# Kernel optimization log

Hardware: AMD Instinct MI355X
Metric: run time of the kernel (lower is better)

The kernel has to match this reference:

```python
import jax, jax.numpy as jnp
import numpy as np

NUM_HEADS = 8
SCALE = 3
TOPKS = [16, 8, 8]  # index 0 = coarsest level


def avg_pool2(t):
    B, C, H, W = t.shape
    return t.reshape(B, C, H // 2, 2, W // 2, 2).mean(axis=(3, 5))


def _to_heads(t, Hi, Wi):
    # [B, C, Hi, Wi] with C = nh*hd (head-major channels) -> [B, nh, Hi*Wi, hd]
    B, C = t.shape[0], t.shape[1]
    hd = C // NUM_HEADS
    return t.reshape(B, NUM_HEADS, hd, Hi * Wi).transpose(0, 1, 3, 2)


def setup_inputs() -> dict:
    key = jax.random.key(0)
    ks = jax.random.split(key, 6)
    B, H, W, C = 2, 96, 96, 128
    N = H * W
    s = 0.02
    return {
        "x": jax.random.normal(ks[0], (B, N, C), jnp.float32),
        "target": jax.random.normal(ks[1], (B, N, C), jnp.float32),
        "Wq": jax.random.normal(ks[2], (C, C), jnp.float32) * s,
        "Wk": jax.random.normal(ks[3], (C, C), jnp.float32) * s,
        "Wv": jax.random.normal(ks[4], (C, C), jnp.float32) * s,
        "Wo": jax.random.normal(ks[5], (C, C), jnp.float32) * s,
        "bo": jnp.zeros((C,), jnp.float32),
        "H": 96,
        "W": 96,
    }


def reference(x, target, Wq, Wk, Wv, Wo, bo, H, W):
    B, N, C = x.shape
    hd = C // NUM_HEADS
    temp = 1.0 / jnp.sqrt(jnp.float32(hd))
    xi = x.transpose(0, 2, 1).reshape(B, C, H, W)
    ti = target.transpose(0, 2, 1).reshape(B, C, H, W)
    # 1x1 conv projections == channel-wise matmul
    q = jnp.einsum('bchw,oc->bohw', xi, Wq)
    k = jnp.einsum('bchw,oc->bohw', ti, Wk)
    v = jnp.einsum('bchw,oc->bohw', ti, Wv)
    qs, ks_, vs, hw = [], [], [], []
    for i in range(SCALE):
        Hi, Wi = H >> i, W >> i
        qs.append(_to_heads(q, Hi, Wi))
        ks_.append(_to_heads(k, Hi, Wi))
        vs.append(_to_heads(v, Hi, Wi))
        hw.append((Hi, Wi))
        if i != SCALE - 1:
            q, k, v = avg_pool2(q), avg_pool2(k), avg_pool2(v)
    # ---- coarsest level: full attention + top-k key selection ----
    i = SCALE - 1
    A = jax.nn.softmax(temp * jnp.einsum('bhnd,bhmd->bhnm', qs[i], ks_[i]), axis=-1)
    msg = jnp.einsum('bhnm,bhmd->bhnd', A, vs[i])  # [B,h,Nc,hd]
    topk_score, topk_idx = jax.lax.top_k(A, TOPKS[0])  # [B,h,Nc,K]
    # ---- refine coarse -> fine over quadtree children of top-k keys ----
    gather = jax.vmap(jax.vmap(lambda arr, idx: arr[idx]))  # over B, h
    for lvl in range(SCALE - 2, -1, -1):
        Hi, Wi = hw[lvl]
        Hp, Wpar = hw[lvl + 1]
        Nf = Hi * Wi
        K = topk_idx.shape[-1]
        yf, xf = jnp.divmod(jnp.arange(Nf), Wi)
        parent = (yf // 2) * Wpar + (xf // 2)  # [Nf] parent query index
        p_idx = topk_idx[:, :, parent, :]  # [B,h,Nf,K] selected coarse keys
        ky, kx = jnp.divmod(p_idx, Wpar)
        dy = jnp.array([0, 0, 1, 1], jnp.int32)
        dx = jnp.array([0, 1, 0, 1], jnp.int32)
        child = ((2 * ky)[..., None] + dy) * Wi + (2 * kx)[..., None] + dx
        cand = child.reshape(B, NUM_HEADS, Nf, K * 4)  # candidate fine keys
        kg = gather(ks_[lvl], cand)  # [B,h,Nf,4K,hd]
        vg = gather(vs[lvl], cand)
        sc = temp * jnp.einsum('bhnd,bhnkd->bhnk', qs[lvl], kg)
        Af = jax.nn.softmax(sc, axis=-1)
        msg_f = jnp.einsum('bhnk,bhnkd->bhnd', Af, vg)
        msg = msg[:, :, parent, :] + msg_f  # assemble with upsampled coarse msg
        if lvl > 0:
            kk = TOPKS[SCALE - 1 - lvl]
            ts, tp = jax.lax.top_k(Af, kk)
            topk_idx = jnp.take_along_axis(cand, tp, axis=-1)
            topk_score = ts
    out = msg.transpose(0, 2, 1, 3).reshape(B, N, C)  # head-major channels
    return out @ Wo.T + bo
```

## Files before the change

### kernel.cpp

```cpp
#include <hip/hip_runtime.h>

#define NB   2
#define NHD  8
#define BH   16
#define HD   16
#define N0   9216
#define N1   2304
#define N2   576
#define W0_  96
#define W1_  48
#define W2_  24
#define M_TOT 18432
#define TEMP 0.25f

__device__ __forceinline__ float kth_largest64(float v, int k){
    unsigned b = __float_as_uint(v);
    unsigned u = (b & 0x80000000u) ? ~b : (b | 0x80000000u);
    unsigned g = 0u;
#pragma unroll
    for(int bit=31; bit>=0; --bit){
        unsigned cand = g | (1u<<bit);
        if ((int)__popcll(__ballot(u >= cand)) >= k) g = cand;
    }
    unsigned rb = (g & 0x80000000u) ? (g & 0x7FFFFFFFu) : ~g;
    return __uint_as_float(rb);
}

__global__ __launch_bounds__(256) void k_proj(const float* __restrict__ x, const float* __restrict__ tg,
    const float* __restrict__ Wq, const float* __restrict__ Wk, const float* __restrict__ Wv,
    float* __restrict__ q0, float* __restrict__ k0, float* __restrict__ v0)
{
    __shared__ __align__(16) float At[16][68];
    __shared__ __align__(16) float Wt[16][132];
    const int t = threadIdx.x;
    const int which = blockIdx.y;
    const float* A  = (which==0)? x : tg;
    const float* Wm = (which==0)? Wq : (which==1? Wk : Wv);
    float* dst      = (which==0)? q0 : (which==1? k0 : v0);
    const int m0 = blockIdx.x * 64;
    const int tx = t & 15, ty = t >> 4;

    float acc[4][8];
#pragma unroll
    for(int i=0;i<4;i++)
#pragma unroll
        for(int j=0;j<8;j++) acc[i][j]=0.f;

    const int ar = t>>2, akq = (t&3)*4;
    const int wo = t>>1, wkq = (t&1)*8;

    for(int kc=0;kc<128;kc+=16){
        float4 av = *(const float4*)(A + (m0+ar)*128 + kc + akq);
        At[akq+0][ar] = av.x;
        At[akq+1][ar] = av.y;
        At[akq+2][ar] = av.z;
        At[akq+3][ar] = av.w;
        float4 w0 = *(const float4*)(Wm + wo*128 + kc + wkq);
        float4 w1 = *(const float4*)(Wm + wo*128 + kc + wkq + 4);
        Wt[wkq+0][wo] = w0.x; Wt[wkq+1][wo] = w0.y;
        Wt[wkq+2][wo] = w0.z; Wt[wkq+3][wo] = w0.w;
        Wt[wkq+4][wo] = w1.x; Wt[wkq+5][wo] = w1.y;
        Wt[wkq+6][wo] = w1.z; Wt[wkq+7][wo] = w1.w;
        __syncthreads();
#pragma unroll
        for(int kk=0;kk<16;kk++){
            float4 a4 = *(const float4*)&At[kk][ty*4];
            float4 wa = *(const float4*)&Wt[kk][tx*4];
            float4 wb = *(const float4*)&Wt[kk][64 + tx*4];
            float avr[4] = {a4.x,a4.y,a4.z,a4.w};
            float wvr[8] = {wa.x,wa.y,wa.z,wa.w, wb.x,wb.y,wb.z,wb.w};
#pragma unroll
            for(int i=0;i<4;i++)
#pragma unroll
                for(int j=0;j<8;j++) acc[i][j] += avr[i]*wvr[j];
        }
        __syncthreads();
    }
    const int hA = tx>>2, dA = (tx&3)*4;
#pragma unroll
    for(int i=0;i<4;i++){
        int m = m0 + ty*4 + i;
        int b = m / N0; int n = m - b*N0;
        float4 sA = make_float4(acc[i][0], acc[i][1], acc[i][2], acc[i][3]);
        float4 sB = make_float4(acc[i][4], acc[i][5], acc[i][6], acc[i][7]);
        *(float4*)(dst + ((b*NHD + hA    )*N0 + n)*16 + dA) = sA;
        *(float4*)(dst + ((b*NHD + hA + 4)*N0 + n)*16 + dA) = sB;
    }
}

__global__ __launch_bounds__(256) void k_pool01(const float4* __restrict__ src0,
    float4* __restrict__ dst1, float4* __restrict__ q2f,
    float4* __restrict__ k2T, float4* __restrict__ v2T)
{
    int tid = blockIdx.x*256 + threadIdx.x;
    if (tid >= 110592) return;
    int d4 = tid & 3;
    int rest = tid >> 2;
    int n2 = rest % N2; int g = rest / N2;
    int yo2 = n2 / W2_, xo2 = n2 - yo2*W2_;

    const float4* s = src0 + g*N0*4;
    float4* d1 = dst1 + g*N1*4;
    float4 l1[4];
#pragma unroll
    for(int yy=0;yy<2;yy++){
#pragma unroll
        for(int xx=0;xx<2;xx++){
            int y1 = 2*yo2+yy, x1 = 2*xo2+xx;
            int n1 = y1*W1_ + x1;
            int cbase = (2*y1)*W0_ + 2*x1;
            float4 a = s[(cbase       )*4 + d4];
            float4 b = s[(cbase+1     )*4 + d4];
            float4 c = s[(cbase+W0_   )*4 + d4];
            float4 d = s[(cbase+W0_+1 )*4 + d4];
            float4 o;
            o.x = 0.25f*(a.x+b.x+c.x+d.x);
            o.y = 0.25f*(a.y+b.y+c.y+d.y);
            o.z = 0.25f*(a.z+b.z+c.z+d.z);
            o.w = 0.25f*(a.w+b.w+c.w+d.w);
            d1[n1*4 + d4] = o;
            l1[yy*2+xx] = o;
        }
    }
    float4 o2;
    o2.x = 0.25f*(l1[0].x+l1[1].x+l1[2].x+l1[3].x);
    o2.y = 0.25f*(l1[0].y+l1[1].y+l1[2].y+l1[3].y);
    o2.z = 0.25f*(l1[0].z+l1[1].z+l1[2].z+l1[3].z);
    o2.w = 0.25f*(l1[0].w+l1[1].w+l1[2].w+l1[3].w);
    int grp = g >> 4, bh = g & 15;
    if (grp == 0)      q2f[(bh*N2 + n2)*4 + d4] = o2;
    else if (grp == 1) k2T[(bh*4 + d4)*N2 + n2] = o2;
    else               v2T[(bh*4 + d4)*N2 + n2] = o2;
}

__device__ __forceinline__ void top16_sel(const float ev[9], int lane, float* cv, int* cx, int* ip)
{
    float head = ev[0];
#pragma unroll
    for(int i=1;i<9;i++) head = fmaxf(head, ev[i]);

    float T = kth_largest64(head, 16);

    int ci = 0;
#pragma unroll
    for(int i=0;i<9;i++) ci += (ev[i] >= T) ? 1 : 0;
    int ps = ci;
#pragma unroll
    for(int d=1;d<64;d<<=1){
        int t = __shfl_up(ps, d);
        if (lane >= d) ps += t;
    }
    int excl = ps - ci;
    int C = __shfl(ps, 63);

    int o = excl;
#pragma unroll
    for(int i=0;i<9;i++){
        if (ev[i] >= T){
            cv[o] = ev[i];
            cx[o] = i*64 + lane;
            o++;
        }
    }
    if (lane < 4){ cv[C+lane] = -1.0f; cx[C+lane] = 0x7fffffff; }

    for(int l=lane; l<C; l+=64){
        float mv = cv[l]; int mi = cx[l];
        int rank = 0;
        for(int c=0;c<C;c+=4){
            float4 vv = *(const float4*)(cv + c);
            int4   ii = *(const int4*)(cx + c);
            rank += (vv.x > mv || (vv.x == mv && ii.x < mi)) ? 1 : 0;
            rank += (vv.y > mv || (vv.y == mv && ii.y < mi)) ? 1 : 0;
            rank += (vv.z > mv || (vv.z == mv && ii.z < mi)) ? 1 : 0;
            rank += (vv.w > mv || (vv.w == mv && ii.w < mi)) ? 1 : 0;
        }
        if (rank < 16) ip[rank] = mi;
    }
}

__global__ __launch_bounds__(256) void k_attn2(const float* __restrict__ q2, const float* __restrict__ k2,
    const float* __restrict__ v2, float* __restrict__ msg2, int* __restrict__ idx2)
{
    __shared__ __align__(16) float cval[4][580];
    __shared__ __align__(16) int   cidx[4][580];
    const int bh = blockIdx.x;
    const int wv = threadIdx.x>>6, lane = threadIdx.x&63;
    const int qA = blockIdx.y*8 + wv*2;
    const int qB = qA + 1;

    float qrA[16], qrB[16];
    {
        const float4* qpA = (const float4*)(q2 + (bh*N2 + qA)*16);
        const float4* qpB = (const float4*)(q2 + (bh*N2 + qB)*16);
#pragma unroll
        for(int dq=0;dq<4;dq++){
            float4 va = qpA[dq];
            qrA[dq*4+0]=va.x; qrA[dq*4+1]=va.y; qrA[dq*4+2]=va.z; qrA[dq*4+3]=va.w;
            float4 vb = qpB[dq];
            qrB[dq*4+0]=vb.x; qrB[dq*4+1]=vb.y; qrB[dq*4+2]=vb.z; qrB[dq*4+3]=vb.w;
        }
    }

    const float4* kT = (const float4*)k2 + bh*4*N2;
    const float4* vT = (const float4*)v2 + bh*4*N2;

    float evA[9], evB[9];
    float mxA = -1e30f, mxB = -1e30f;
#pragma unroll
    for(int t9=0;t9<9;t9++){
        int m = t9*64 + lane;
        float sA = 0.f, sB = 0.f;
#pragma unroll
        for(int dg=0;dg<4;dg++){
            float4 kv = kT[dg*N2 + m];
            sA += qrA[dg*4+0]*kv.x + qrA[dg*4+1]*kv.y + qrA[dg*4+2]*kv.z + qrA[dg*4+3]*kv.w;
            sB += qrB[dg*4+0]*kv.x + qrB[dg*4+1]*kv.y + qrB[dg*4+2]*kv.z + qrB[dg*4+3]*kv.w;
        }
        sA *= TEMP; sB *= TEMP;
        evA[t9]=sA; evB[t9]=sB;
        mxA = fmaxf(mxA, sA);
        mxB = fmaxf(mxB, sB);
    }
#pragma unroll
    for(int st=1; st<64; st<<=1){
        mxA = fmaxf(mxA, __shfl_xor(mxA, st));
        mxB = fmaxf(mxB, __shfl_xor(mxB, st));
    }

    float sumA=0.f, sumB=0.f;
    float accA[16], accB[16];
#pragma unroll
    for(int d=0;d<16;d++){ accA[d]=0.f; accB[d]=0.f; }
#pragma unroll
    for(int t9=0;t9<9;t9++){
        int m = t9*64 + lane;
        float eA = expf(evA[t9]-mxA);
        float eB = expf(evB[t9]-mxB);
        evA[t9]=eA; evB[t9]=eB;
        sumA += eA; sumB += eB;
#pragma unroll
        for(int dg=0;dg<4;dg++){
            float4 vv = vT[dg*N2 + m];
            accA[dg*4+0] += eA*vv.x; accA[dg*4+1] += eA*vv.y;
            accA[dg*4+2] += eA*vv.z; accA[dg*4+3] += eA*vv.w;
            accB[dg*4+0] += eB*vv.x; accB[dg*4+1] += eB*vv.y;
            accB[dg*4+2] += eB*vv.z; accB[dg*4+3] += eB*vv.w;
        }
    }
#pragma unroll
    for(int st=1; st<64; st<<=1){
        sumA += __shfl_xor(sumA, st);
        sumB += __shfl_xor(sumB, st);
    }

    const bool b5 = (lane & 32) != 0;
    const bool b4 = (lane & 16) != 0;
    const bool b3 = (lane & 8) != 0;
    const bool b2 = (lane & 4) != 0;
    float r8A[8], r8B[8];
#pragma unroll
    for(int i=0;i<8;i++){
        float sndA  = b5 ? accA[i]   : accA[i+8];
        float keptA = b5 ? accA[i+8] : accA[i];
        r8A[i] = keptA + __shfl_xor(sndA, 32);
        float sndB  = b5 ? accB[i]   : accB[i+8];
        float keptB = b5 ? accB[i+8] : accB[i];
        r8B[i] = keptB + __shfl_xor(sndB, 32);
    }
    float r4A[4], r4B[4];
#pragma unroll
    for(int i=0;i<4;i++){
        float sndA  = b4 ? r8A[i]   : r8A[i+4];
        float keptA = b4 ? r8A[i+4] : r8A[i];
        r4A[i] = keptA + __shfl_xor(sndA, 16);
        float sndB  = b4 ? r8B[i]   : r8B[i+4];
        float keptB = b4 ? r8B[i+4] : r8B[i];
        r4B[i] = keptB + __shfl_xor(sndB, 16);
    }
    float r2A[2], r2B[2];
#pragma unroll
    for(int i=0;i<2;i++){
        float sndA  = b3 ? r4A[i]   : r4A[i+2];
        float keptA = b3 ? r4A[i+2] : r4A[i];
        r2A[i] = keptA + __shfl_xor(sndA, 8);
        float sndB  = b3 ? r4B[i]   : r4B[i+2];
        float keptB = b3 ? r4B[i+2] : r4B[i];
        r2B[i] = keptB + __shfl_xor(sndB, 8);
    }
    {
        float sndA  = b2 ? r2A[0] : r2A[1];
        float keptA = b2 ? r2A[1] : r2A[0];
        r2A[0] = keptA + __shfl_xor(sndA, 4);
        float sndB  = b2 ? r2B[0] : r2B[1];
        float keptB = b2 ? r2B[1] : r2B[0];
        r2B[0] = keptB + __shfl_xor(sndB, 4);
    }
    r2A[0] += __shfl_xor(r2A[0], 2);
    r2B[0] += __shfl_xor(r2B[0], 2);
    r2A[0] += __shfl_xor(r2A[0], 1);
    r2B[0] += __shfl_xor(r2B[0], 1);
    float invA = 1.0f/sumA, invB = 1.0f/sumB;
    if ((lane&3)==0){
        msg2[(bh*N2+qA)*16 + (lane>>2)] = r2A[0]*invA;
        msg2[(bh*N2+qB)*16 + (lane>>2)] = r2B[0]*invB;
    }

    top16_sel(evA, lane, cval[wv], cidx[wv], idx2 + (bh*N2+qA)*16);
    top16_sel(evB, lane, cval[wv], cidx[wv], idx2 + (bh*N2+qB)*16);
}

__global__ __launch_bounds__(256) void k_ref10(
    const float* __restrict__ q1, const float* __restrict__ k1, const float* __restrict__ v1,
    const float* __restrict__ q0, const float* __restrict__ k0, const float* __restrict__ v0,
    const float* __restrict__ msg2, const int* __restrict__ idx2, float* __restrict__ msg0)
{
    __shared__ float msg1s[4][16];
    __shared__ int   idx1s[4][8];
    const int bid = (blockIdx.x & 7)*1152 + (blockIdx.x >> 3);
    const int bh = bid / 576, tile = bid - bh*576;
    const int tyy = tile / 24, txx = tile - tyy*24;
    const int py0 = tyy*2, px0 = txx*2;
    const int wv = threadIdx.x>>6, lane = threadIdx.x&63;

    const int ppy = py0 + (wv>>1), ppx = px0 + (wv&1);

    {
        const int n  = ppy*W1_ + ppx;
        const int par = (ppy>>1)*W2_ + (ppx>>1);
        const int kk = lane>>2, tt = lane&3, dy = tt>>1, dx = tt&1;
        int p = idx2[(bh*N2+par)*16 + kk];
        int ky = p / W2_, kx = p - ky*W2_;
        int child = (2*ky+dy)*W1_ + 2*kx+dx;

        const float* qp = q1 + (bh*N1+n)*16;
        float qr[16];
#pragma unroll
        for(int d=0; d<16; d+=4){
            float4 qq = *(const float4*)(qp+d);
            qr[d]=qq.x; qr[d+1]=qq.y; qr[d+2]=qq.z; qr[d+3]=qq.w;
        }
        const float4* kp = (const float4*)(k1 + (bh*N1+child)*16);
        float s = 0.f;
#pragma unroll
        for(int dq=0;dq<4;dq++){
            float4 kv = kp[dq];
            s += qr[dq*4+0]*kv.x + qr[dq*4+1]*kv.y + qr[dq*4+2]*kv.z + qr[dq*4+3]*kv.w;
        }
        s *= TEMP;

        float T8 = kth_largest64(s, 8);
        unsigned long long mgt = __ballot(s > T8);
        unsigned long long meq = __ballot(s == T8);
        int ngt = (int)__popcll(mgt);
        int ltg = __builtin_amdgcn_mbcnt_lo((unsigned)mgt, 0);
        ltg = __builtin_amdgcn_mbcnt_hi((unsigned)(mgt>>32), ltg);
        int lte = __builtin_amdgcn_mbcnt_lo((unsigned)meq, 0);
        lte = __builtin_amdgcn_mbcnt_hi((unsigned)(meq>>32), lte);
        int slot = (s > T8) ? ltg : ((s == T8) ? (ngt + lte) : 8);
        if (slot < 8) idx1s[wv][slot] = child;

        float e = expf(s);
        float sum = e;
#pragma unroll
        for(int st=1; st<64; st<<=1) sum += __shfl_xor(sum, st);

        float acc[16];
        const float4* vp = (const float4*)(v1 + (bh*N1+child)*16);
#pragma unroll
        for(int dq=0;dq<4;dq++){
            float4 vv = vp[dq];
            acc[dq*4+0]=e*vv.x; acc[dq*4+1]=e*vv.y; acc[dq*4+2]=e*vv.z; acc[dq*4+3]=e*vv.w;
        }
        const bool b5 = (lane & 32) != 0;
        float r8[8];
#pragma unroll
        for(int ii=0;ii<8;ii++){
            float snd  = b5 ? acc[ii]   : acc[ii+8];
            float kept = b5 ? acc[ii+8] : acc[ii];
            r8[ii] = kept + __shfl_xor(snd, 32);
        }
        const bool b4 = (lane & 16) != 0;
        float r4[4];
#pragma unroll
        for(int ii=0;ii<4;ii++){
            float snd  = b4 ? r8[ii]   : r8[ii+4];
            float kept = b4 ? r8[ii+4] : r8[ii];
            r4[ii] = kept + __shfl_xor(snd, 16);
        }
        const bool b3 = (lane & 8) != 0;
        float r2[2];
#pragma unroll
        for(int ii=0;ii<2;ii++){
            float snd  = b3 ? r4[ii]   : r4[ii+2];
            float kept = b3 ? r4[ii+2] : r4[ii];
            r2[ii] = kept + __shfl_xor(snd, 8);
        }
        const bool b2 = (lane & 4) != 0;
        {
            float snd  = b2 ? r2[0] : r2[1];
            float kept = b2 ? r2[1] : r2[0];
            r2[0] = kept + __shfl_xor(snd, 4);
        }
        r2[0] += __shfl_xor(r2[0], 2);
        r2[0] += __shfl_xor(r2[0], 1);

        float inv1 = 1.0f/sum;
        if ((lane&3)==0){
            int d = lane>>2;
            msg1s[wv][d] = msg2[(bh*N2+par)*16 + d] + r2[0]*inv1;
        }
    }

    const int j = lane & 31, sub = lane >> 5;
    const int kk = j>>2, tt = j&3, dy = tt>>1, dx = tt&1;
    int p = idx1s[wv][kk];
    int ky = p / W1_, kx = p - ky*W1_;
    int child = (2*ky+dy)*W0_ + 2*kx+dx;

    float kr[16];
    {
        const float4* kp = (const float4*)(k0 + (bh*N0+child)*16);
#pragma unroll
        for(int dq=0;dq<4;dq++){
            float4 kv = kp[dq];
            kr[dq*4+0]=kv.x; kr[dq*4+1]=kv.y; kr[dq*4+2]=kv.z; kr[dq*4+3]=kv.w;
        }
    }
    const int cy0 = 2*ppy, cx0 = 2*ppx + sub;
    int nq[2];
    float s_[2];
#pragma unroll
    for(int it=0; it<2; it++){
        nq[it] = (cy0+it)*W0_ + cx0;
        const float* qp = q0 + (bh*N0+nq[it])*16;
        float qr[16];
#pragma unroll
        for(int d=0; d<16; d+=4){
            float4 qq = *(const float4*)(qp+d);
            qr[d]=qq.x; qr[d+1]=qq.y; qr[d+2]=qq.z; qr[d+3]=qq.w;
        }
        float s = 0.f;
#pragma unroll
        for(int dq=0;dq<4;dq++){
            s += qr[dq*4+0]*kr[dq*4+0] + qr[dq*4+1]*kr[dq*4+1]
               + qr[dq*4+2]*kr[dq*4+2] + qr[dq*4+3]*kr[dq*4+3];
        }
        s_[it] = s * TEMP;
    }
    float vr[16];
    {
        const float4* vp = (const float4*)(v0 + (bh*N0+child)*16);
#pragma unroll
        for(int dq=0;dq<4;dq++){
            float4 vv = vp[dq];
            vr[dq*4+0]=vv.x; vr[dq*4+1]=vv.y; vr[dq*4+2]=vv.z; vr[dq*4+3]=vv.w;
        }
    }
    const float m1d = msg1s[wv][j>>1];

    float e0 = expf(s_[0]);
    float e1 = expf(s_[1]);
    float sum0 = e0, sum1 = e1;
#pragma unroll
    for(int st=1; st<32; st<<=1){
        sum0 += __shfl_xor(sum0, st);
        sum1 += __shfl_xor(sum1, st);
    }

    float acc0[16], acc1[16];
#pragma unroll
    for(int d=0;d<16;d++){ acc0[d] = e0*vr[d]; acc1[d] = e1*vr[d]; }

    const bool c4 = (j & 16) != 0;
    float p8A[8], p8B[8];
#pragma unroll
    for(int ii=0;ii<8;ii++){
        float sndA  = c4 ? acc0[ii]   : acc0[ii+8];
        float keptA = c4 ? acc0[ii+8] : acc0[ii];
        p8A[ii] = keptA + __shfl_xor(sndA, 16);
        float sndB  = c4 ? acc1[ii]   : acc1[ii+8];
        float keptB = c4 ? acc1[ii+8] : acc1[ii];
        p8B[ii] = keptB + __shfl_xor(sndB, 16);
    }
    const bool c3 = (j & 8) != 0;
    float p4A[4], p4B[4];
#pragma unroll
    for(int ii=0;ii<4;ii++){
        float sndA  = c3 ? p8A[ii]   : p8A[ii+4];
        float keptA = c3 ? p8A[ii+4] : p8A[ii];
        p4A[ii] = keptA + __shfl_xor(sndA, 8);
        float sndB  = c3 ? p8B[ii]   : p8B[ii+4];
        float keptB = c3 ? p8B[ii+4] : p8B[ii];
        p4B[ii] = keptB + __shfl_xor(sndB, 8);
    }
    const bool c2 = (j & 4) != 0;
    float p2A[2], p2B[2];
#pragma unroll
    for(int ii=0;ii<2;ii++){
        float sndA  = c2 ? p4A[ii]   : p4A[ii+2];
        float keptA = c2 ? p4A[ii+2] : p4A[ii];
        p2A[ii] = keptA + __shfl_xor(sndA, 4);
        float sndB  = c2 ? p4B[ii]   : p4B[ii+2];
        float keptB = c2 ? p4B[ii+2] : p4B[ii];
        p2B[ii] = keptB + __shfl_xor(sndB, 4);
    }
    const bool c1 = (j & 2) != 0;
    {
        float sndA  = c1 ? p2A[0] : p2A[1];
        float keptA = c1 ? p2A[1] : p2A[0];
        p2A[0] = keptA + __shfl_xor(sndA, 2);
        float sndB  = c1 ? p2B[0] : p2B[1];
        float keptB = c1 ? p2B[1] : p2B[0];
        p2B[0] = keptB + __shfl_xor(sndB, 2);
    }
    p2A[0] += __shfl_xor(p2A[0], 1);
    p2B[0] += __shfl_xor(p2B[0], 1);

    float inv0 = 1.0f/sum0, inv1 = 1.0f/sum1;
    if ((j&1)==0){
        int d = j>>1;
        int b_ = bh>>3, h = bh&7;
        msg0[(b_*N0+nq[0])*128 + h*16 + d] = m1d + p2A[0]*inv0;
        msg0[(b_*N0+nq[1])*128 + h*16 + d] = m1d + p2B[0]*inv1;
    }
}

__global__ __launch_bounds__(256) void k_out(const float* __restrict__ msg0, const float* __restrict__ Wo,
    const float* __restrict__ bo, float* __restrict__ out)
{
    __shared__ __align__(16) float At[16][68];
    __shared__ __align__(16) float Wt[16][132];
    const int t = threadIdx.x;
    const int m0 = blockIdx.x * 64;
    const int tx = t & 15, ty = t >> 4;

    float acc[4][8];
#pragma unroll
    for(int i=0;i<4;i++)
#pragma unroll
        for(int j=0;j<8;j++) acc[i][j]=0.f;

    const int ar = t>>2, akq = (t&3)*4;
    const int wo = t>>1, wkq = (t&1)*8;

    for(int kc=0;kc<128;kc+=16){
        float4 av = *(const float4*)(msg0 + (m0+ar)*128 + kc + akq);
        At[akq+0][ar] = av.x;
        At[akq+1][ar] = av.y;
        At[akq+2][ar] = av.z;
        At[akq+3][ar] = av.w;
        float4 w0 = *(const float4*)(Wo + wo*128 + kc + wkq);
        float4 w1 = *(const float4*)(Wo + wo*128 + kc + wkq + 4);
        Wt[wkq+0][wo] = w0.x; Wt[wkq+1][wo] = w0.y;
        Wt[wkq+2][wo] = w0.z; Wt[wkq+3][wo] = w0.w;
        Wt[wkq+4][wo] = w1.x; Wt[wkq+5][wo] = w1.y;
        Wt[wkq+6][wo] = w1.z; Wt[wkq+7][wo] = w1.w;
        __syncthreads();
#pragma unroll
        for(int kk=0;kk<16;kk++){
            float4 a4 = *(const float4*)&At[kk][ty*4];
            float4 wa = *(const float4*)&Wt[kk][tx*4];
            float4 wb = *(const float4*)&Wt[kk][64 + tx*4];
            float avr[4] = {a4.x,a4.y,a4.z,a4.w};
            float wvr[8] = {wa.x,wa.y,wa.z,wa.w, wb.x,wb.y,wb.z,wb.w};
#pragma unroll
            for(int i=0;i<4;i++)
#pragma unroll
                for(int j=0;j<8;j++) acc[i][j] += avr[i]*wvr[j];
        }
        __syncthreads();
    }
#pragma unroll
    for(int i=0;i<4;i++){
        int m = m0 + ty*4 + i;
        float4 sA = make_float4(acc[i][0]+bo[tx*4+0], acc[i][1]+bo[tx*4+1],
                                acc[i][2]+bo[tx*4+2], acc[i][3]+bo[tx*4+3]);
        float4 sB = make_float4(acc[i][4]+bo[64+tx*4+0], acc[i][5]+bo[64+tx*4+1],
                                acc[i][6]+bo[64+tx*4+2], acc[i][7]+bo[64+tx*4+3]);
        *(float4*)(out + m*128 + tx*4)      = sA;
        *(float4*)(out + m*128 + 64 + tx*4) = sB;
    }
}

extern "C" void kernel_launch(void* const* d_in, const int* in_sizes, int n_in,
                              void* d_out, int out_size, void* d_ws, size_t ws_size,
                              hipStream_t stream) {
    const float* x  = (const float*)d_in[0];
    const float* tg = (const float*)d_in[1];
    const float* Wq = (const float*)d_in[2];
    const float* Wk = (const float*)d_in[3];
    const float* Wv = (const float*)d_in[4];
    const float* Wo = (const float*)d_in[5];
    const float* bo = (const float*)d_in[6];

    float* ws = (float*)d_ws;
    float* q0   = ws + 0;
    float* k0   = ws + 2359296;
    float* v0   = ws + 4718592;
    float* q1   = ws + 7077888;
    float* k1   = ws + 7667712;
    float* v1   = ws + 8257536;
    float* q2   = ws + 8847360;
    float* k2   = ws + 8994816;
    float* v2   = ws + 9142272;
    float* msg2 = ws + 9289728;
    float* msg0 = ws + 10027008;
    int*   idx2 = (int*)(ws + 12386304);

    k_proj<<<dim3(288,3), 256, 0, stream>>>(x, tg, Wq, Wk, Wv, q0, k0, v0);
    k_pool01<<<432, 256, 0, stream>>>((const float4*)q0, (float4*)q1,
                                      (float4*)q2, (float4*)k2, (float4*)v2);
    k_attn2<<<dim3(16,72), 256, 0, stream>>>(q2, k2, v2, msg2, idx2);
    k_ref10<<<9216, 256, 0, stream>>>(q1, k1, v1, q0, k0, v0, msg2, idx2, msg0);
    k_out<<<288, 256, 0, stream>>>(msg0, Wo, bo, (float*)d_out);
}
```

Measured before the change: 214.6 us.

## Prefetch GEMM tiles into registers, ballot-based prefix scan, fast exp

The projection and output GEMM kernels now load the next k-chunk of A and W into registers before computing on the current shared-memory tile, so global load latency overlaps with the FMA loop. The shuffle-based inclusive scan in top-16 selection is replaced by four ballot/mbcnt steps over the count bits. expf calls in the fine-level attention kernels become __expf, which is faster but less accurate. The prefetch adds register pressure, and the bitwise scan assumes per-lane counts below 16.

```diff
diff --git a/kernel.cpp b/kernel.cpp
--- a/kernel.cpp
+++ b/kernel.cpp
@@ -24,6 +24,18 @@
     }
     unsigned rb = (g & 0x80000000u) ? (g & 0x7FFFFFFFu) : ~g;
     return __uint_as_float(rb);
+}
+
+__device__ __forceinline__ void scan_counts64(int ci, int &excl, int &C){
+    excl = 0; C = 0;
+#pragma unroll
+    for(int b=0;b<4;b++){
+        unsigned long long mb = __ballot(((unsigned)ci>>b)&1u);
+        int lt = __builtin_amdgcn_mbcnt_lo((unsigned)mb, 0);
+        lt = __builtin_amdgcn_mbcnt_hi((unsigned)(mb>>32), lt);
+        excl += lt << b;
+        C += ((int)__popcll(mb)) << b;
+    }
 }
 
 __global__ __launch_bounds__(256) void k_proj(const float* __restrict__ x, const float* __restrict__ tg,
@@ -49,19 +61,26 @@
     const int ar = t>>2, akq = (t&3)*4;
     const int wo = t>>1, wkq = (t&1)*8;
 
+    float4 av = *(const float4*)(A + (m0+ar)*128 + akq);
+    float4 w0 = *(const float4*)(Wm + wo*128 + wkq);
+    float4 w1 = *(const float4*)(Wm + wo*128 + wkq + 4);
+
     for(int kc=0;kc<128;kc+=16){
-        float4 av = *(const float4*)(A + (m0+ar)*128 + kc + akq);
         At[akq+0][ar] = av.x;
         At[akq+1][ar] = av.y;
         At[akq+2][ar] = av.z;
         At[akq+3][ar] = av.w;
-        float4 w0 = *(const float4*)(Wm + wo*128 + kc + wkq);
-        float4 w1 = *(const float4*)(Wm + wo*128 + kc + wkq + 4);
         Wt[wkq+0][wo] = w0.x; Wt[wkq+1][wo] = w0.y;
         Wt[wkq+2][wo] = w0.z; Wt[wkq+3][wo] = w0.w;
         Wt[wkq+4][wo] = w1.x; Wt[wkq+5][wo] = w1.y;
         Wt[wkq+6][wo] = w1.z; Wt[wkq+7][wo] = w1.w;
         __syncthreads();
+        float4 nav, nw0, nw1;
+        if (kc < 112){
+            nav = *(const float4*)(A + (m0+ar)*128 + kc+16 + akq);
+            nw0 = *(const float4*)(Wm + wo*128 + kc+16 + wkq);
+            nw1 = *(const float4*)(Wm + wo*128 + kc+16 + wkq + 4);
+        }
 #pragma unroll
         for(int kk=0;kk<16;kk++){
             float4 a4 = *(const float4*)&At[kk][ty*4];
@@ -75,6 +94,7 @@
                 for(int j=0;j<8;j++) acc[i][j] += avr[i]*wvr[j];
         }
         __syncthreads();
+        if (kc < 112){ av = nav; w0 = nw0; w1 = nw1; }
     }
     const int hA = tx>>2, dA = (tx&3)*4;
 #pragma unroll
@@ -144,14 +164,8 @@
     int ci = 0;
 #pragma unroll
     for(int i=0;i<9;i++) ci += (ev[i] >= T) ? 1 : 0;
-    int ps = ci;
-#pragma unroll
-    for(int d=1;d<64;d<<=1){
-        int t = __shfl_up(ps, d);
-        if (lane >= d) ps += t;
-    }
-    int excl = ps - ci;
-    int C = __shfl(ps, 63);
+    int excl, C;
+    scan_counts64(ci, excl, C);
 
     int o = excl;
 #pragma unroll
@@ -360,7 +374,7 @@
         int slot = (s > T8) ? ltg : ((s == T8) ? (ngt + lte) : 8);
         if (slot < 8) idx1s[wv][slot] = child;
 
-        float e = expf(s);
+        float e = __expf(s);
         float sum = e;
 #pragma unroll
         for(int st=1; st<64; st<<=1) sum += __shfl_xor(sum, st);
@@ -459,8 +473,8 @@
     }
     const float m1d = msg1s[wv][j>>1];
 
-    float e0 = expf(s_[0]);
-    float e1 = expf(s_[1]);
+    float e0 = __expf(s_[0]);
+    float e1 = __expf(s_[1]);
     float sum0 = e0, sum1 = e1;
 #pragma unroll
     for(int st=1; st<32; st<<=1){
@@ -544,19 +558,26 @@
     const int ar = t>>2, akq = (t&3)*4;
     const int wo = t>>1, wkq = (t&1)*8;
 
+    float4 av = *(const float4*)(msg0 + (m0+ar)*128 + akq);
+    float4 w0 = *(const float4*)(Wo + wo*128 + wkq);
+    float4 w1 = *(const float4*)(Wo + wo*128 + wkq + 4);
+
     for(int kc=0;kc<128;kc+=16){
-        float4 av = *(const float4*)(msg0 + (m0+ar)*128 + kc + akq);
         At[akq+0][ar] = av.x;
         At[akq+1][ar] = av.y;
         At[akq+2][ar] = av.z;
         At[akq+3][ar] = av.w;
-        float4 w0 = *(const float4*)(Wo + wo*128 + kc + wkq);
-        float4 w1 = *(const float4*)(Wo + wo*128 + kc + wkq + 4);
         Wt[wkq+0][wo] = w0.x; Wt[wkq+1][wo] = w0.y;
         Wt[wkq+2][wo] = w0.z; Wt[wkq+3][wo] = w0.w;
         Wt[wkq+4][wo] = w1.x; Wt[wkq+5][wo] = w1.y;
         Wt[wkq+6][wo] = w1.z; Wt[wkq+7][wo] = w1.w;
         __syncthreads();
+        float4 nav, nw0, nw1;
+        if (kc < 112){
+            nav = *(const float4*)(msg0 + (m0+ar)*128 + kc+16 + akq);
+            nw0 = *(const float4*)(Wo + wo*128 + kc+16 + wkq);
+            nw1 = *(const float4*)(Wo + wo*128 + kc+16 + wkq + 4);
+        }
 #pragma unroll
         for(int kk=0;kk<16;kk++){
             float4 a4 = *(const float4*)&At[kk][ty*4];
@@ -570,6 +591,7 @@
                 for(int j=0;j<8;j++) acc[i][j] += avr[i]*wvr[j];
         }
         __syncthreads();
+        if (kc < 112){ av = nav; w0 = nw0; w1 = nw1; }
     }
 #pragma unroll
     for(int i=0;i<4;i++){
```

After: 218.2 us. Within noise of the previous version (+1.7%).
